# Kernel optimization log

Hardware: AMD Instinct MI355X
Metric: run time of the kernel (lower is better)

Reference implementation:

```python
import jax, jax.numpy as jnp
import numpy as np

B, N, M = 4, 2048, 2048
QD, CD = 1024, 768
H, DH = 8, 64
INNER = H * DH  # 512


def setup_inputs() -> dict:
    key = jax.random.key(0)
    ks = jax.random.split(key, 6)
    s = 0.02
    return {
        "x": jax.random.normal(ks[0], (B, N, QD), dtype=jnp.float32),
        "context": jax.random.normal(ks[1], (B, M, CD), dtype=jnp.float32),
        "Wq": jax.random.normal(ks[2], (QD, INNER), dtype=jnp.float32) * s,
        "Wk": jax.random.normal(ks[3], (CD, INNER), dtype=jnp.float32) * s,
        "Wv": jax.random.normal(ks[4], (CD, INNER), dtype=jnp.float32) * s,
        "Wo": jax.random.normal(ks[5], (INNER, QD), dtype=jnp.float32) * s,
        "bo": jnp.zeros((QD,), dtype=jnp.float32),
    }


def reference(x, context, Wq, Wk, Wv, Wo, bo):
    scale = DH ** (-0.5)
    b, n, _ = x.shape
    m = context.shape[1]
    # projections (no bias, as in torch module)
    q = (x @ Wq).reshape(b, n, H, DH)        # b n h d
    k = (context @ Wk).reshape(b, m, H, DH)  # b m h d
    v = (context @ Wv).reshape(b, m, H, DH)
    # scaled dot-product attention, full materialized scores (faithful to source)
    sim = jnp.einsum("bihd,bjhd->bhij", q, k) * scale  # [b,h,n,m]
    attn = jax.nn.softmax(sim, axis=-1)
    out = jnp.einsum("bhij,bjhd->bihd", attn, v).reshape(b, n, INNER)
    return out @ Wo + bo
```

## Files before the change

kernel.cpp:

```cpp
#include <hip/hip_runtime.h>
#include <cstdint>
#include <cstddef>


typedef __bf16 bf16;
typedef __bf16 bf16x8 __attribute__((ext_vector_type(8)));
typedef __bf16 bf16x4 __attribute__((ext_vector_type(4)));
typedef float  f32x4  __attribute__((ext_vector_type(4)));
typedef float  f32x16 __attribute__((ext_vector_type(16)));

#define B_     4
#define N_     2048
#define M_     2048
#define QD_    1024
#define CD_    768
#define H_     8
#define DH_    64
#define INNER_ 512

__device__ __forceinline__ void gload_lds16(const void* g, void* l) {
  __builtin_amdgcn_global_load_lds(
      (__attribute__((address_space(1))) unsigned int*)g,
      (__attribute__((address_space(3))) unsigned int*)l, 16, 0, 0);
}

__global__ __launch_bounds__(256) void k_cvt(const float* __restrict__ in,
                                             bf16* __restrict__ out) {
  int i = blockIdx.x * 256 + threadIdx.x;
  float4 v = reinterpret_cast<const float4*>(in)[i];
  bf16x4 o;
  o[0] = (bf16)v.x; o[1] = (bf16)v.y; o[2] = (bf16)v.z; o[3] = (bf16)v.w;
  reinterpret_cast<bf16x4*>(out)[i] = o;
}

__global__ __launch_bounds__(256) void k_wT(const float* __restrict__ in,
                                            bf16* __restrict__ out, int K, int N) {
  int t = blockIdx.x * 256 + threadIdx.x;
  int n = t / K, k = t - n * K;
  out[t] = (bf16)in[(size_t)k * N + n];
}

__global__ __launch_bounds__(256) void k_vT(const bf16* __restrict__ V,
                                            bf16* __restrict__ VT) {
  int t = blockIdx.x * 256 + threadIdx.x;
  int m = t & (M_ - 1);
  int rest = t >> 11;
  int d = rest & 63;
  int bh = rest >> 6;
  VT[t] = V[((size_t)((bh >> 3) * M_ + m)) * INNER_ + (bh & 7) * DH_ + d];
}

__device__ __forceinline__ void gemm_core(
    const bf16* __restrict__ A, const bf16* __restrict__ BT,
    bf16* __restrict__ Cb, float* __restrict__ Cf, const float* __restrict__ bias,
    int Kdim, int Ndim, float alpha) {
  __shared__ char lds[16384];
  const int t = threadIdx.x;
  const int wid = t >> 6, l = t & 63, g = l >> 4, r16 = l & 15;
  const int wr = wid >> 1, wc = wid & 1;
  const int m0 = blockIdx.x * 128, n0 = blockIdx.y * 128;

  f32x4 acc[4][4];
#pragma unroll
  for (int ai = 0; ai < 4; ++ai)
#pragma unroll
    for (int bj = 0; bj < 4; ++bj) acc[ai][bj] = (f32x4){0.f, 0.f, 0.f, 0.f};

  const int rS = t >> 2;
  const int lsS = (t & 3) ^ ((rS >> 1) & 3);
  const size_t a0 = (size_t)(m0 + rS) * Kdim + lsS * 8;
  const size_t a1 = (size_t)(m0 + 64 + rS) * Kdim + lsS * 8;
  const size_t b0 = (size_t)(n0 + rS) * Kdim + lsS * 8;
  const size_t b1 = (size_t)(n0 + 64 + rS) * Kdim + lsS * 8;
  char* ldsA = lds;
  char* ldsB = lds + 8192;

  for (int k0 = 0; k0 < Kdim; k0 += 32) {
    __syncthreads();
    gload_lds16(A + a0 + k0, ldsA + wid * 1024);
    gload_lds16(A + a1 + k0, ldsA + 4096 + wid * 1024);
    gload_lds16(BT + b0 + k0, ldsB + wid * 1024);
    gload_lds16(BT + b1 + k0, ldsB + 4096 + wid * 1024);
    __syncthreads();

    bf16x8 af[4], bfr[4];
#pragma unroll
    for (int i = 0; i < 4; ++i) {
      const int rowA = wr * 64 + i * 16 + r16;
      af[i] = *reinterpret_cast<const bf16x8*>(
          ldsA + rowA * 64 + ((g ^ ((rowA >> 1) & 3)) << 4));
      const int rowB = wc * 64 + i * 16 + r16;
      bfr[i] = *reinterpret_cast<const bf16x8*>(
          ldsB + rowB * 64 + ((g ^ ((rowB >> 1) & 3)) << 4));
    }
#pragma unroll
    for (int ai = 0; ai < 4; ++ai)
#pragma unroll
      for (int bj = 0; bj < 4; ++bj)
        acc[ai][bj] = __builtin_amdgcn_mfma_f32_16x16x32_bf16(
            af[ai], bfr[bj], acc[ai][bj], 0, 0, 0);
  }

#pragma unroll
  for (int ai = 0; ai < 4; ++ai)
#pragma unroll
    for (int bj = 0; bj < 4; ++bj)
#pragma unroll
      for (int r = 0; r < 4; ++r) {
        const int row = m0 + wr * 64 + ai * 16 + g * 4 + r;
        const int col = n0 + wc * 64 + bj * 16 + r16;
        const float v = acc[ai][bj][r] * alpha;
        if (Cf) Cf[(size_t)row * Ndim + col] = v + bias[col];
        else    Cb[(size_t)row * Ndim + col] = (bf16)v;
      }
}

__global__ __launch_bounds__(256) void k_gemm_qkv(
    const bf16* __restrict__ xb, const bf16* __restrict__ cb,
    const bf16* __restrict__ WqT, const bf16* __restrict__ WkT,
    const bf16* __restrict__ WvT,
    bf16* __restrict__ Q, bf16* __restrict__ K, bf16* __restrict__ V) {
  const int z = blockIdx.z;
  gemm_core(z == 0 ? xb : cb,
            z == 0 ? WqT : (z == 1 ? WkT : WvT),
            z == 0 ? Q : (z == 1 ? K : V),
            nullptr, nullptr,
            z == 0 ? QD_ : CD_, INNER_,
            z == 0 ? 0.125f : 1.0f);
}

__global__ __launch_bounds__(256) void k_gemm_out(
    const bf16* __restrict__ AO, const bf16* __restrict__ WoT,
    float* __restrict__ Cout, const float* __restrict__ bias) {
  gemm_core(AO, WoT, nullptr, Cout, bias, INNER_, QD_, 1.0f);
}

__global__ __launch_bounds__(256) void k_attn(const bf16* __restrict__ Qg,
                                              const bf16* __restrict__ Kg,
                                              const bf16* __restrict__ VTg,
                                              bf16* __restrict__ AO) {
  __shared__ char lds[33280];
  const int t = threadIdx.x;
  const int w = t >> 6, l = t & 63;
  const int ql = l & 31, h5 = l >> 5;
  const int h = blockIdx.y, b = blockIdx.z;
  const int q0 = blockIdx.x * 128 + w * 32;

  const bf16* qbase =
      Qg + ((size_t)(b * N_ + q0 + ql)) * INNER_ + h * DH_ + 8 * h5;
  bf16x8 qf[4];
#pragma unroll
  for (int j = 0; j < 4; ++j)
    qf[j] = *reinterpret_cast<const bf16x8*>(qbase + 16 * j);

  f32x16 o0, o1;
#pragma unroll
  for (int i = 0; i < 16; ++i) { o0[i] = 0.f; o1[i] = 0.f; }
  float m_run = -1e30f, l_run = 0.f;

  const int rstg = t >> 3;
  const int ls = (t & 7) ^ (rstg & 7);
  const int prow = (rstg & ~12) | ((rstg & 4) << 1) | ((rstg & 8) >> 1);
  const size_t kbase = (size_t)(b * M_) * INNER_ + h * DH_;
  const size_t vbase = (size_t)((b * H_ + h) * DH_) * (size_t)M_;

#define STAGE(bi, mm)                                                          \
  {                                                                            \
    char* Kd = lds + (bi)*16384;                                               \
    char* Vd = Kd + 8192;                                                      \
    gload_lds16(Kg + kbase + (size_t)((mm) + prow) * INNER_ + ls * 8,          \
                Kd + w * 1024);                                                \
    gload_lds16(Kg + kbase + (size_t)((mm) + 32 + prow) * INNER_ + ls * 8,     \
                Kd + 4096 + w * 1024);                                         \
    gload_lds16(VTg + vbase + (size_t)rstg * M_ + (mm) + ls * 8,               \
                Vd + w * 1024);                                                \
    gload_lds16(VTg + vbase + (size_t)(32 + rstg) * M_ + (mm) + ls * 8,        \
                Vd + 4096 + w * 1024);                                         \
  }

  STAGE(0, 0)
  __syncthreads();

  for (int mt = 0; mt < M_ / 64; ++mt) {
    const int cur = mt & 1;
    if (mt + 1 < M_ / 64) STAGE(cur ^ 1, (mt + 1) * 64)
    const char* Kl = lds + cur * 16384;
    const char* Vl = Kl + 8192;

    f32x16 s0, s1;
#pragma unroll
    for (int i = 0; i < 16; ++i) { s0[i] = 0.f; s1[i] = 0.f; }
#pragma unroll
    for (int j = 0; j < 4; ++j) {
      const int sw = ((2 * j + h5) ^ (ql & 7)) << 4;
      const bf16x8 ka0 = *reinterpret_cast<const bf16x8*>(Kl + ql * 128 + sw);
      s0 = __builtin_amdgcn_mfma_f32_32x32x16_bf16(ka0, qf[j], s0, 0, 0, 0);
      const bf16x8 ka1 =
          *reinterpret_cast<const bf16x8*>(Kl + (ql + 32) * 128 + sw);
      s1 = __builtin_amdgcn_mfma_f32_32x32x16_bf16(ka1, qf[j], s1, 0, 0, 0);
    }

    float mx = s0[0];
#pragma unroll
    for (int i = 1; i < 16; ++i) mx = fmaxf(mx, s0[i]);
#pragma unroll
    for (int i = 0; i < 16; ++i) mx = fmaxf(mx, s1[i]);
    mx = fmaxf(mx, __shfl_xor(mx, 32, 64));
    if (!__all(mx <= m_run + 8.0f)) {
      const float mnew = fmaxf(m_run, mx);
      const float corr = __expf(m_run - mnew);
#pragma unroll
      for (int i = 0; i < 16; ++i) { o0[i] *= corr; o1[i] *= corr; }
      l_run *= corr;
      m_run = mnew;
    }
    float rs = 0.f;
#pragma unroll
    for (int i = 0; i < 16; ++i) { s0[i] = __expf(s0[i] - m_run); rs += s0[i]; }
#pragma unroll
    for (int i = 0; i < 16; ++i) { s1[i] = __expf(s1[i] - m_run); rs += s1[i]; }
    rs += __shfl_xor(rs, 32, 64);
    l_run += rs;

    bf16x8 pa[4];
#pragma unroll
    for (int c = 0; c < 4; ++c)
#pragma unroll
      for (int j2 = 0; j2 < 8; ++j2)
        pa[c][j2] = (bf16)((c >> 1) ? s1[8 * (c & 1) + j2]
                                    : s0[8 * (c & 1) + j2]);

#pragma unroll
    for (int c = 0; c < 4; ++c) {
      const int sw = ((2 * c + h5) ^ (ql & 7)) << 4;
      const bf16x8 vb0 = *reinterpret_cast<const bf16x8*>(Vl + ql * 128 + sw);
      o0 = __builtin_amdgcn_mfma_f32_32x32x16_bf16(pa[c], vb0, o0, 0, 0, 0);
      const bf16x8 vb1 =
          *reinterpret_cast<const bf16x8*>(Vl + (ql + 32) * 128 + sw);
      o1 = __builtin_amdgcn_mfma_f32_32x32x16_bf16(pa[c], vb1, o1, 0, 0, 0);
    }
    __syncthreads();
  }
#undef STAGE

  float* linv = reinterpret_cast<float*>(lds + 32768) + w * 32;
  if (h5 == 0) linv[ql] = 1.0f / l_run;
  __syncthreads();
#pragma unroll
  for (int r = 0; r < 16; ++r) {
    const int qrow = (r & 3) + 8 * (r >> 2) + 4 * h5;
    const float inv = linv[qrow];
    const size_t base = ((size_t)(b * N_ + q0 + qrow)) * INNER_ + h * DH_;
    AO[base + ql] = (bf16)(o0[r] * inv);
    AO[base + 32 + ql] = (bf16)(o1[r] * inv);
  }
}

extern "C" void kernel_launch(void* const* d_in, const int* in_sizes, int n_in,
                              void* d_out, int out_size, void* d_ws, size_t ws_size,
                              hipStream_t stream) {
  const float* x   = (const float*)d_in[0];
  const float* ctx = (const float*)d_in[1];
  const float* Wq  = (const float*)d_in[2];
  const float* Wk  = (const float*)d_in[3];
  const float* Wv  = (const float*)d_in[4];
  const float* Wo  = (const float*)d_in[5];
  const float* bo  = (const float*)d_in[6];
  float* out = (float*)d_out;

  char* ws = (char*)d_ws;
  bf16* xb  = (bf16*)ws; ws += (size_t)B_ * N_ * QD_ * 2;
  bf16* cb  = (bf16*)ws; ws += (size_t)B_ * M_ * CD_ * 2;
  bf16* WqT = (bf16*)ws; ws += (size_t)QD_ * INNER_ * 2;
  bf16* WkT = (bf16*)ws; ws += (size_t)CD_ * INNER_ * 2;
  bf16* WvT = (bf16*)ws; ws += (size_t)CD_ * INNER_ * 2;
  bf16* WoT = (bf16*)ws; ws += (size_t)INNER_ * QD_ * 2;
  bf16* Qb  = (bf16*)ws; ws += (size_t)B_ * N_ * INNER_ * 2;
  bf16* Kb  = (bf16*)ws; ws += (size_t)B_ * M_ * INNER_ * 2;
  bf16* Vb  = (bf16*)ws; ws += (size_t)B_ * M_ * INNER_ * 2;
  bf16* VTb = (bf16*)ws; ws += (size_t)B_ * M_ * INNER_ * 2;
  bf16* AOb = (bf16*)ws; ws += (size_t)B_ * N_ * INNER_ * 2;

  k_cvt<<<(B_ * N_ * QD_) / 1024, 256, 0, stream>>>(x, xb);
  k_cvt<<<(B_ * M_ * CD_) / 1024, 256, 0, stream>>>(ctx, cb);
  k_wT<<<(QD_ * INNER_) / 256, 256, 0, stream>>>(Wq, WqT, QD_, INNER_);
  k_wT<<<(CD_ * INNER_) / 256, 256, 0, stream>>>(Wk, WkT, CD_, INNER_);
  k_wT<<<(CD_ * INNER_) / 256, 256, 0, stream>>>(Wv, WvT, CD_, INNER_);
  k_wT<<<(INNER_ * QD_) / 256, 256, 0, stream>>>(Wo, WoT, INNER_, QD_);

  k_gemm_qkv<<<dim3(64, 4, 3), 256, 0, stream>>>(xb, cb, WqT, WkT, WvT,
                                                 Qb, Kb, Vb);
  k_vT<<<(B_ * H_ * DH_ * M_) / 256, 256, 0, stream>>>(Vb, VTb);
  k_attn<<<dim3(N_ / 128, H_, B_), 256, 0, stream>>>(Qb, Kb, VTb, AOb);
  k_gemm_out<<<dim3(64, 8), 256, 0, stream>>>(AOb, WoT, out, bo);
}
```

Measured before the change: 251.3 us.

## Fuse V transpose into QKV GEMM, double-buffer GEMM, retune attention softmax

The V transpose kernel is removed: the QKV GEMM epilogue writes V directly in transposed layout, saving a launch and a round trip through memory. The GEMM gains a double-buffered LDS pipeline. The attention kernel moves to 128-thread blocks with smaller query tiles. It folds log2(e) into the Q scale so it can use raw v_exp_f32, computes the row sum with an extra MFMA against ones, and uses full-wave max reduction, a lazy rescale threshold and s_setprio around the MFMA sections. The transposed epilogue stores are scattered, and the extra MFMA adds matrix work.

```diff
diff --git a/kernel.cpp b/kernel.cpp
--- a/kernel.cpp
+++ b/kernel.cpp
@@ -24,6 +24,12 @@
       (__attribute__((address_space(3))) unsigned int*)l, 16, 0, 0);
 }
 
+__device__ __forceinline__ float exp2_fast(float x) {
+  float r;
+  asm("v_exp_f32 %0, %1" : "=v"(r) : "v"(x));
+  return r;
+}
+
 __global__ __launch_bounds__(256) void k_cvt(const float* __restrict__ in,
                                              bf16* __restrict__ out) {
   int i = blockIdx.x * 256 + threadIdx.x;
@@ -40,21 +46,11 @@
   out[t] = (bf16)in[(size_t)k * N + n];
 }
 
-__global__ __launch_bounds__(256) void k_vT(const bf16* __restrict__ V,
-                                            bf16* __restrict__ VT) {
-  int t = blockIdx.x * 256 + threadIdx.x;
-  int m = t & (M_ - 1);
-  int rest = t >> 11;
-  int d = rest & 63;
-  int bh = rest >> 6;
-  VT[t] = V[((size_t)((bh >> 3) * M_ + m)) * INNER_ + (bh & 7) * DH_ + d];
-}
-
 __device__ __forceinline__ void gemm_core(
     const bf16* __restrict__ A, const bf16* __restrict__ BT,
-    bf16* __restrict__ Cb, float* __restrict__ Cf, const float* __restrict__ bias,
-    int Kdim, int Ndim, float alpha) {
-  __shared__ char lds[16384];
+    bf16* __restrict__ Cb, bf16* __restrict__ Cvt, float* __restrict__ Cf,
+    const float* __restrict__ bias, int Kdim, int Ndim, float alpha) {
+  __shared__ char lds[32768];
   const int t = threadIdx.x;
   const int wid = t >> 6, l = t & 63, g = l >> 4, r16 = l & 15;
   const int wr = wid >> 1, wc = wid & 1;
@@ -72,16 +68,26 @@
   const size_t a1 = (size_t)(m0 + 64 + rS) * Kdim + lsS * 8;
   const size_t b0 = (size_t)(n0 + rS) * Kdim + lsS * 8;
   const size_t b1 = (size_t)(n0 + 64 + rS) * Kdim + lsS * 8;
-  char* ldsA = lds;
-  char* ldsB = lds + 8192;
-
-  for (int k0 = 0; k0 < Kdim; k0 += 32) {
-    __syncthreads();
-    gload_lds16(A + a0 + k0, ldsA + wid * 1024);
-    gload_lds16(A + a1 + k0, ldsA + 4096 + wid * 1024);
-    gload_lds16(BT + b0 + k0, ldsB + wid * 1024);
-    gload_lds16(BT + b1 + k0, ldsB + 4096 + wid * 1024);
-    __syncthreads();
+
+#define GSTAGE(bi, kk)                                                         \
+  {                                                                            \
+    char* ldsA = lds + (bi)*16384;                                             \
+    char* ldsB = ldsA + 8192;                                                  \
+    gload_lds16(A + a0 + (kk), ldsA + wid * 1024);                             \
+    gload_lds16(A + a1 + (kk), ldsA + 4096 + wid * 1024);                      \
+    gload_lds16(BT + b0 + (kk), ldsB + wid * 1024);                            \
+    gload_lds16(BT + b1 + (kk), ldsB + 4096 + wid * 1024);                     \
+  }
+
+  GSTAGE(0, 0)
+  __syncthreads();
+
+  const int nk = Kdim >> 5;
+  for (int kt = 0; kt < nk; ++kt) {
+    const int cur = kt & 1;
+    if (kt + 1 < nk) GSTAGE(cur ^ 1, (kt + 1) * 32)
+    const char* ldsA = lds + cur * 16384;
+    const char* ldsB = ldsA + 8192;
 
     bf16x8 af[4], bfr[4];
 #pragma unroll
@@ -99,7 +105,9 @@
       for (int bj = 0; bj < 4; ++bj)
         acc[ai][bj] = __builtin_amdgcn_mfma_f32_16x16x32_bf16(
             af[ai], bfr[bj], acc[ai][bj], 0, 0, 0);
-  }
+    __syncthreads();
+  }
+#undef GSTAGE
 
 #pragma unroll
   for (int ai = 0; ai < 4; ++ai)
@@ -110,8 +118,16 @@
         const int row = m0 + wr * 64 + ai * 16 + g * 4 + r;
         const int col = n0 + wc * 64 + bj * 16 + r16;
         const float v = acc[ai][bj][r] * alpha;
-        if (Cf) Cf[(size_t)row * Ndim + col] = v + bias[col];
-        else    Cb[(size_t)row * Ndim + col] = (bf16)v;
+        if (Cf) {
+          Cf[(size_t)row * Ndim + col] = v + bias[col];
+        } else if (Cvt) {
+          const size_t vt =
+              (((size_t)(row >> 11) * 8 + (col >> 6)) * 64 + (col & 63)) * M_ +
+              (row & (M_ - 1));
+          Cvt[vt] = (bf16)v;
+        } else {
+          Cb[(size_t)row * Ndim + col] = (bf16)v;
+        }
       }
 }
 
@@ -119,32 +135,33 @@
     const bf16* __restrict__ xb, const bf16* __restrict__ cb,
     const bf16* __restrict__ WqT, const bf16* __restrict__ WkT,
     const bf16* __restrict__ WvT,
-    bf16* __restrict__ Q, bf16* __restrict__ K, bf16* __restrict__ V) {
+    bf16* __restrict__ Q, bf16* __restrict__ K, bf16* __restrict__ VT) {
   const int z = blockIdx.z;
   gemm_core(z == 0 ? xb : cb,
             z == 0 ? WqT : (z == 1 ? WkT : WvT),
-            z == 0 ? Q : (z == 1 ? K : V),
+            z == 0 ? Q : K,
+            z == 2 ? VT : nullptr,
             nullptr, nullptr,
             z == 0 ? QD_ : CD_, INNER_,
-            z == 0 ? 0.125f : 1.0f);
+            z == 0 ? 0.18033688f  : 1.0f);
 }
 
 __global__ __launch_bounds__(256) void k_gemm_out(
     const bf16* __restrict__ AO, const bf16* __restrict__ WoT,
     float* __restrict__ Cout, const float* __restrict__ bias) {
-  gemm_core(AO, WoT, nullptr, Cout, bias, INNER_, QD_, 1.0f);
-}
-
-__global__ __launch_bounds__(256) void k_attn(const bf16* __restrict__ Qg,
+  gemm_core(AO, WoT, nullptr, nullptr, Cout, bias, INNER_, QD_, 1.0f);
+}
+
+__global__ __launch_bounds__(128) void k_attn(const bf16* __restrict__ Qg,
                                               const bf16* __restrict__ Kg,
                                               const bf16* __restrict__ VTg,
                                               bf16* __restrict__ AO) {
-  __shared__ char lds[33280];
+  __shared__ char lds[32768];
   const int t = threadIdx.x;
   const int w = t >> 6, l = t & 63;
   const int ql = l & 31, h5 = l >> 5;
   const int h = blockIdx.y, b = blockIdx.z;
-  const int q0 = blockIdx.x * 128 + w * 32;
+  const int q0 = blockIdx.x * 64 + w * 32;
 
   const bf16* qbase =
       Qg + ((size_t)(b * N_ + q0 + ql)) * INNER_ + h * DH_ + 8 * h5;
@@ -153,14 +170,18 @@
   for (int j = 0; j < 4; ++j)
     qf[j] = *reinterpret_cast<const bf16x8*>(qbase + 16 * j);
 
-  f32x16 o0, o1;
-#pragma unroll
-  for (int i = 0; i < 16; ++i) { o0[i] = 0.f; o1[i] = 0.f; }
-  float m_run = -1e30f, l_run = 0.f;
+  bf16x8 onesf;
+#pragma unroll
+  for (int j = 0; j < 8; ++j) onesf[j] = (bf16)1.0f;
+
+  f32x16 o0, o1, lA;
+#pragma unroll
+  for (int i = 0; i < 16; ++i) { o0[i] = 0.f; o1[i] = 0.f; lA[i] = 0.f; }
+  float m_run = -1e30f;
 
   const int rstg = t >> 3;
   const int ls = (t & 7) ^ (rstg & 7);
-  const int prow = (rstg & ~12) | ((rstg & 4) << 1) | ((rstg & 8) >> 1);
+  const int perm = (rstg & 3) | ((rstg & 4) << 1) | ((rstg & 8) >> 1);
   const size_t kbase = (size_t)(b * M_) * INNER_ + h * DH_;
   const size_t vbase = (size_t)((b * H_ + h) * DH_) * (size_t)M_;
 
@@ -168,14 +189,13 @@
   {                                                                            \
     char* Kd = lds + (bi)*16384;                                               \
     char* Vd = Kd + 8192;                                                      \
-    gload_lds16(Kg + kbase + (size_t)((mm) + prow) * INNER_ + ls * 8,          \
-                Kd + w * 1024);                                                \
-    gload_lds16(Kg + kbase + (size_t)((mm) + 32 + prow) * INNER_ + ls * 8,     \
-                Kd + 4096 + w * 1024);                                         \
-    gload_lds16(VTg + vbase + (size_t)rstg * M_ + (mm) + ls * 8,               \
-                Vd + w * 1024);                                                \
-    gload_lds16(VTg + vbase + (size_t)(32 + rstg) * M_ + (mm) + ls * 8,        \
-                Vd + 4096 + w * 1024);                                         \
+    _Pragma("unroll") for (int rr = 0; rr < 4; ++rr) {                         \
+      gload_lds16(Kg + kbase + (size_t)((mm) + rr * 16 + perm) * INNER_ +      \
+                      ls * 8,                                                  \
+                  Kd + rr * 2048 + w * 1024);                                  \
+      gload_lds16(VTg + vbase + (size_t)(rr * 16 + rstg) * M_ + (mm) + ls * 8, \
+                  Vd + rr * 2048 + w * 1024);                                  \
+    }                                                                          \
   }
 
   STAGE(0, 0)
@@ -190,6 +210,7 @@
     f32x16 s0, s1;
 #pragma unroll
     for (int i = 0; i < 16; ++i) { s0[i] = 0.f; s1[i] = 0.f; }
+    __builtin_amdgcn_s_setprio(1);
 #pragma unroll
     for (int j = 0; j < 4; ++j) {
       const int sw = ((2 * j + h5) ^ (ql & 7)) << 4;
@@ -199,57 +220,56 @@
           *reinterpret_cast<const bf16x8*>(Kl + (ql + 32) * 128 + sw);
       s1 = __builtin_amdgcn_mfma_f32_32x32x16_bf16(ka1, qf[j], s1, 0, 0, 0);
     }
-
-    float mx = s0[0];
-#pragma unroll
-    for (int i = 1; i < 16; ++i) mx = fmaxf(mx, s0[i]);
-#pragma unroll
-    for (int i = 0; i < 16; ++i) mx = fmaxf(mx, s1[i]);
-    mx = fmaxf(mx, __shfl_xor(mx, 32, 64));
-    if (!__all(mx <= m_run + 8.0f)) {
-      const float mnew = fmaxf(m_run, mx);
-      const float corr = __expf(m_run - mnew);
-#pragma unroll
-      for (int i = 0; i < 16; ++i) { o0[i] *= corr; o1[i] *= corr; }
-      l_run *= corr;
-      m_run = mnew;
+    __builtin_amdgcn_s_setprio(0);
+
+    float mx = fmaxf(fmaxf(s0[0], s0[1]), fmaxf(s0[2], s0[3]));
+#pragma unroll
+    for (int i = 4; i < 16; i += 3)
+      mx = fmaxf(fmaxf(mx, s0[i]), fmaxf(s0[i + 1], s0[i + 2]));
+#pragma unroll
+    for (int i = 0; i < 16; i += 4)
+      mx = fmaxf(fmaxf(mx, s1[i]),
+                 fmaxf(fmaxf(s1[i + 1], s1[i + 2]), s1[i + 3]));
+#pragma unroll
+    for (int off = 1; off <= 32; off <<= 1)
+      mx = fmaxf(mx, __shfl_xor(mx, off, 64));
+    if (mx > m_run + 11.5f) {
+      const float corr = exp2_fast(m_run - mx);
+#pragma unroll
+      for (int i = 0; i < 16; ++i) {
+        o0[i] *= corr; o1[i] *= corr; lA[i] *= corr;
+      }
+      m_run = mx;
     }
-    float rs = 0.f;
-#pragma unroll
-    for (int i = 0; i < 16; ++i) { s0[i] = __expf(s0[i] - m_run); rs += s0[i]; }
-#pragma unroll
-    for (int i = 0; i < 16; ++i) { s1[i] = __expf(s1[i] - m_run); rs += s1[i]; }
-    rs += __shfl_xor(rs, 32, 64);
-    l_run += rs;
-
-    bf16x8 pa[4];
-#pragma unroll
-    for (int c = 0; c < 4; ++c)
+#pragma unroll
+    for (int i = 0; i < 16; ++i) s0[i] = exp2_fast(s0[i] - m_run);
+#pragma unroll
+    for (int i = 0; i < 16; ++i) s1[i] = exp2_fast(s1[i] - m_run);
+
+    __builtin_amdgcn_s_setprio(1);
+#pragma unroll
+    for (int c = 0; c < 4; ++c) {
+      bf16x8 pa;
 #pragma unroll
       for (int j2 = 0; j2 < 8; ++j2)
-        pa[c][j2] = (bf16)((c >> 1) ? s1[8 * (c & 1) + j2]
-                                    : s0[8 * (c & 1) + j2]);
-
-#pragma unroll
-    for (int c = 0; c < 4; ++c) {
+        pa[j2] = (bf16)((c >= 2) ? s1[8 * (c & 1) + j2] : s0[8 * (c & 1) + j2]);
       const int sw = ((2 * c + h5) ^ (ql & 7)) << 4;
       const bf16x8 vb0 = *reinterpret_cast<const bf16x8*>(Vl + ql * 128 + sw);
-      o0 = __builtin_amdgcn_mfma_f32_32x32x16_bf16(pa[c], vb0, o0, 0, 0, 0);
+      o0 = __builtin_amdgcn_mfma_f32_32x32x16_bf16(pa, vb0, o0, 0, 0, 0);
       const bf16x8 vb1 =
           *reinterpret_cast<const bf16x8*>(Vl + (ql + 32) * 128 + sw);
-      o1 = __builtin_amdgcn_mfma_f32_32x32x16_bf16(pa[c], vb1, o1, 0, 0, 0);
+      o1 = __builtin_amdgcn_mfma_f32_32x32x16_bf16(pa, vb1, o1, 0, 0, 0);
+      lA = __builtin_amdgcn_mfma_f32_32x32x16_bf16(pa, onesf, lA, 0, 0, 0);
     }
+    __builtin_amdgcn_s_setprio(0);
     __syncthreads();
   }
 #undef STAGE
 
-  float* linv = reinterpret_cast<float*>(lds + 32768) + w * 32;
-  if (h5 == 0) linv[ql] = 1.0f / l_run;
-  __syncthreads();
 #pragma unroll
   for (int r = 0; r < 16; ++r) {
+    const float inv = __builtin_amdgcn_rcpf(lA[r]);
     const int qrow = (r & 3) + 8 * (r >> 2) + 4 * h5;
-    const float inv = linv[qrow];
     const size_t base = ((size_t)(b * N_ + q0 + qrow)) * INNER_ + h * DH_;
     AO[base + ql] = (bf16)(o0[r] * inv);
     AO[base + 32 + ql] = (bf16)(o1[r] * inv);
@@ -277,7 +297,6 @@
   bf16* WoT = (bf16*)ws; ws += (size_t)INNER_ * QD_ * 2;
   bf16* Qb  = (bf16*)ws; ws += (size_t)B_ * N_ * INNER_ * 2;
   bf16* Kb  = (bf16*)ws; ws += (size_t)B_ * M_ * INNER_ * 2;
-  bf16* Vb  = (bf16*)ws; ws += (size_t)B_ * M_ * INNER_ * 2;
   bf16* VTb = (bf16*)ws; ws += (size_t)B_ * M_ * INNER_ * 2;
   bf16* AOb = (bf16*)ws; ws += (size_t)B_ * N_ * INNER_ * 2;
 
@@ -289,8 +308,7 @@
   k_wT<<<(INNER_ * QD_) / 256, 256, 0, stream>>>(Wo, WoT, INNER_, QD_);
 
   k_gemm_qkv<<<dim3(64, 4, 3), 256, 0, stream>>>(xb, cb, WqT, WkT, WvT,
-                                                 Qb, Kb, Vb);
-  k_vT<<<(B_ * H_ * DH_ * M_) / 256, 256, 0, stream>>>(Vb, VTb);
-  k_attn<<<dim3(N_ / 128, H_, B_), 256, 0, stream>>>(Qb, Kb, VTb, AOb);
+                                                 Qb, Kb, VTb);
+  k_attn<<<dim3(N_ / 64, H_, B_), 128, 0, stream>>>(Qb, Kb, VTb, AOb);
   k_gemm_out<<<dim3(64, 8), 256, 0, stream>>>(AOb, WoT, out, bo);
 }
```

Measured after the change: 248.3 us. About the same (-1.2%).
